# Optimization experiments

Hardware: AMD Instinct MI355X
Metric: run time of the kernel (lower is better)

Reference implementation:

```python
import jax, jax.numpy as jnp
import numpy as np

NUMBASIS = 10
OFFSET = jnp.linspace(-3.0, 3.0, NUMBASIS)
COEFF = -0.5 / (OFFSET[1] - OFFSET[0]) ** 2
CR_CR_MEAN, CR_CR_STD = 4.0, 0.16
CR_I_MEAN, CR_I_STD = 2.8, 0.035
ANGLE_MEAN, ANGLE_STD = -0.025, 0.06

E, N, G = 1_000_000, 250_000, 512

def _rbf(x):
    # x: [E, 1] -> [E, NUMBASIS]; PyG GaussianSmearing
    d = x - OFFSET
    return jnp.exp(COEFF * d * d)

def _layernorm(x, g, b, eps=1e-5):
    mu = jnp.mean(x, axis=-1, keepdims=True)
    xc = x - mu
    var = jnp.mean(xc * xc, axis=-1, keepdims=True)
    return xc * jax.lax.rsqrt(var + eps) * g + b

def setup_inputs() -> dict:
    key = jax.random.key(0)
    ks = jax.random.split(key, 16)
    def w(k, shape):
        return jax.random.normal(k, shape, jnp.float32) / np.sqrt(shape[0])
    return {
        "edge_src": jax.random.randint(ks[0], (E,), 0, N),
        "edge_dst": jax.random.randint(ks[1], (E,), 0, N),
        "batch_idx": jnp.sort(jax.random.randint(ks[2], (N,), 0, G)),
        "cell": jax.random.normal(ks[3], (G, 3, 3), jnp.float32),
        "edge_shift": jax.random.normal(ks[4], (E, 3), jnp.float32),
        "pos": jax.random.normal(ks[5], (N, 3), jnp.float32),
        "angles": jax.random.normal(ks[6], (E,), jnp.float32),
        "cr_i_bonds": jax.random.normal(ks[7], (E, 4), jnp.float32),
        "ln_g": jnp.ones((60,), jnp.float32),
        "ln_b": jnp.zeros((60,), jnp.float32),
        "wn1": w(ks[8], (60, 32)), "bn1": jnp.zeros((32,), jnp.float32),
        "wn2": w(ks[9], (32, 1)), "bn2": jnp.zeros((1,), jnp.float32),
        "we1": w(ks[10], (60, 64)), "be1": jnp.zeros((64,), jnp.float32),
        "we2": w(ks[11], (64, 1)), "be2": jnp.zeros((1,), jnp.float32),
        "wr1": w(ks[12], (60, 32)), "br1": jnp.zeros((32,), jnp.float32),
        "wr2": w(ks[13], (32, 2)), "br2": jnp.zeros((2,), jnp.float32),
    }

def reference(edge_src, edge_dst, batch_idx, cell, edge_shift, pos, angles,
              cr_i_bonds, ln_g, ln_b, wn1, bn1, wn2, bn2, we1, be1, we2, be2,
              wr1, br1, wr2, br2):
    gidx = batch_idx[edge_src]                      # [E]
    bcell = cell[gidx]                              # [E,3,3]
    tvec = jnp.einsum('ei,eij->ej', edge_shift, bcell)
    radvec = pos[edge_dst] - pos[edge_src] + tvec   # [E,3]
    dist = jnp.linalg.norm(radvec, axis=1, keepdims=True)  # [E,1]
    ang = angles.reshape(-1, 1)
    dist_z = (dist - CR_CR_MEAN) / CR_CR_STD
    ang_z = (ang - ANGLE_MEAN) / ANGLE_STD
    legs_z = (cr_i_bonds - CR_I_MEAN) / CR_I_STD    # [E,4]
    emb = jnp.concatenate([
        _rbf(dist_z), _rbf(ang_z),
        _rbf(legs_z[:, 0:1]), _rbf(legs_z[:, 1:2]),
        _rbf(legs_z[:, 2:3]), _rbf(legs_z[:, 3:4]),
    ], axis=-1)                                     # [E,60]
    h = _layernorm(emb, ln_g, ln_b)
    # dropout layers are identity in eval mode
    routing = jax.nn.softmax(jax.nn.silu(h @ wr1 + br1) @ wr2 + br2, axis=-1)
    pred_normal = jax.nn.silu(h @ wn1 + bn1) @ wn2 + bn2   # [E,1]
    pred_extreme = jax.nn.silu(h @ we1 + be1) @ we2 + be2  # [E,1]
    out = routing[:, 0:1] * pred_normal + routing[:, 1:2] * pred_extreme
    return out.reshape(-1)
```

## Files before the change

### kernel.cpp

```cpp
#include <hip/hip_runtime.h>
#include <math.h>

#define E_THREADS 256
#define EPB 256

typedef __attribute__((ext_vector_type(8))) short short8;
typedef __attribute__((ext_vector_type(4))) float floatx4;


__device__ __constant__ float c_B[10] = {
    -9.7397680f, -7.5753751f, -5.4109822f, -3.2465893f, -1.0821964f,
     1.0821964f,  3.2465893f,  5.4109822f,  7.5753751f,  9.7397680f
};
__device__ __constant__ float c_C[10] = {
    -14.609652f, -8.8378534f, -4.5091519f, -1.6232946f, -0.18036607f,
    -0.18036607f, -1.6232946f, -4.5091519f, -8.8378534f, -14.609652f
};

__device__ inline unsigned short f2bf(float f) {
    union { float f; unsigned u; } v; v.f = f;
    unsigned r = v.u + 0x7FFFu + ((v.u >> 16) & 1u);
    return (unsigned short)(r >> 16);
}

__device__ inline unsigned cvt_pk_bf16(float lo, float hi) {
    unsigned r;
    asm("v_cvt_pk_bf16_f32 %0, %1, %2" : "=v"(r) : "v"(lo), "v"(hi));
    return r;
}

__device__ inline float fexp2(float x) { return __builtin_amdgcn_exp2f(x); }
__device__ inline float frcp(float x)  { return __builtin_amdgcn_rcpf(x); }
#define LOG2E 1.44269504f

__global__ __launch_bounds__(256)
void prep_weights(
    const float* __restrict__ ln_g, const float* __restrict__ ln_b,
    const float* __restrict__ wn1, const float* __restrict__ bn1,
    const float* __restrict__ wn2, const float* __restrict__ bn2,
    const float* __restrict__ we1, const float* __restrict__ be1,
    const float* __restrict__ we2, const float* __restrict__ be2,
    const float* __restrict__ wr1, const float* __restrict__ br1,
    const float* __restrict__ wr2, const float* __restrict__ br2,
    char* __restrict__ ws)
{
    uint4* WF  = (uint4*)ws;
    float* W2A = (float*)(ws + 16384);
    float* W2B = (float*)(ws + 16896);
    float* SC  = (float*)(ws + 17024);
    const int tid = threadIdx.x;

    for (int idx = tid; idx < 1024; idx += 256) {
        int u = idx >> 7, s = (idx >> 6) & 1, lane = idx & 63;
        int lcol = lane & 15, khi = lane >> 4;
        int n = 16 * u + lcol;
        int kbase = s * 32 + khi * 8;
        float w8[8];
        for (int j = 0; j < 8; ++j) {
            int k = kbase + j;
            float w = 0.0f;
            if (k < 60) {
                float wv = (n < 32) ? wn1[k * 32 + n]
                         : (n < 96) ? we1[k * 64 + (n - 32)]
                                    : wr1[k * 32 + (n - 96)];
                w = ln_g[k] * wv;
            } else if (k == 60) {
                float b = (n < 32) ? bn1[n] : (n < 96) ? be1[n - 32] : br1[n - 96];
                for (int kk = 0; kk < 60; ++kk) {
                    float wv = (n < 32) ? wn1[kk * 32 + n]
                             : (n < 96) ? we1[kk * 64 + (n - 32)]
                                        : wr1[kk * 32 + (n - 96)];
                    b += ln_b[kk] * wv;
                }
                w = b;
            }
            w8[j] = w;
        }
        unsigned q0 = (unsigned)f2bf(w8[0]) | ((unsigned)f2bf(w8[1]) << 16);
        unsigned q1 = (unsigned)f2bf(w8[2]) | ((unsigned)f2bf(w8[3]) << 16);
        unsigned q2 = (unsigned)f2bf(w8[4]) | ((unsigned)f2bf(w8[5]) << 16);
        unsigned q3 = (unsigned)f2bf(w8[6]) | ((unsigned)f2bf(w8[7]) << 16);
        WF[idx] = make_uint4(q0, q1, q2, q3);
    }
    if (tid < 128) {
        int n = tid;
        W2A[n] = (n < 32) ? wn2[n] : (n < 96) ? we2[n - 32] : wr2[(n - 96) * 2];
    }
    if (tid >= 128 && tid < 160) W2B[tid - 128] = wr2[(tid - 128) * 2 + 1];
    if (tid == 0) { SC[0] = bn2[0]; SC[1] = be2[0]; SC[2] = br2[0]; SC[3] = br2[1]; }
}

__attribute__((amdgpu_waves_per_eu(4, 4)))
__global__ __launch_bounds__(E_THREADS, 4)
void exchange_block_kernel(
    const int*   __restrict__ edge_src,
    const int*   __restrict__ edge_dst,
    const int*   __restrict__ batch_idx,
    const float* __restrict__ cell,
    const float* __restrict__ edge_shift,
    const float* __restrict__ pos,
    const float* __restrict__ angles,
    const float* __restrict__ cr_bonds,
    const char*  __restrict__ ws,
    float* __restrict__ out, int E)
{
    __shared__ __align__(16) unsigned short HLDS[EPB * 64];
    __shared__ __align__(16) float LW2A[128];
    __shared__ __align__(16) float LW2B[32];

    const int tid = threadIdx.x;
    const int e = blockIdx.x * EPB + tid;

    if (tid < 128)                LW2A[tid] = ((const float*)(ws + 16384))[tid];
    else if (tid < 160)           LW2B[tid - 128] = ((const float*)(ws + 16896))[tid - 128];

    float h[64];
    if (e < E) {
        int s = edge_src[e];
        int d = edge_dst[e];
        int g = batch_idx[s];
        float sh0 = edge_shift[e * 3 + 0];
        float sh1 = edge_shift[e * 3 + 1];
        float sh2 = edge_shift[e * 3 + 2];
        const float* c = cell + g * 9;
        float t0 = sh0 * c[0] + sh1 * c[3] + sh2 * c[6];
        float t1 = sh0 * c[1] + sh1 * c[4] + sh2 * c[7];
        float t2 = sh0 * c[2] + sh1 * c[5] + sh2 * c[8];
        float r0 = pos[d * 3 + 0] - pos[s * 3 + 0] + t0;
        float r1 = pos[d * 3 + 1] - pos[s * 3 + 1] + t1;
        float r2 = pos[d * 3 + 2] - pos[s * 3 + 2] + t2;
        float dist = sqrtf(r0 * r0 + r1 * r1 + r2 * r2);

        float z[6];
        z[0] = (dist - 4.0f) * (1.0f / 0.16f);
        z[1] = (angles[e] + 0.025f) * (1.0f / 0.06f);
        z[2] = (cr_bonds[e * 4 + 0] - 2.8f) * (1.0f / 0.035f);
        z[3] = (cr_bonds[e * 4 + 1] - 2.8f) * (1.0f / 0.035f);
        z[4] = (cr_bonds[e * 4 + 2] - 2.8f) * (1.0f / 0.035f);
        z[5] = (cr_bonds[e * 4 + 3] - 2.8f) * (1.0f / 0.035f);

        #pragma unroll
        for (int gi = 0; gi < 6; ++gi) {
            float zv = z[gi];
            float az2 = -1.6232946f * zv * zv;
            #pragma unroll
            for (int k = 0; k < 10; ++k)
                h[gi * 10 + k] = fexp2(az2 + fmaf(zv, c_B[k], c_C[k]));
        }
        float mu = 0.0f;
        #pragma unroll
        for (int k = 0; k < 60; ++k) mu += h[k];
        mu *= (1.0f / 60.0f);
        float var = 0.0f;
        #pragma unroll
        for (int k = 0; k < 60; ++k) { float xc = h[k] - mu; var += xc * xc; }
        var *= (1.0f / 60.0f);
        float rs = rsqrtf(var + 1e-5f);
        float nmurs = -mu * rs;
        #pragma unroll
        for (int k = 0; k < 60; ++k) h[k] = fmaf(h[k], rs, nmurs);
    } else {
        #pragma unroll
        for (int k = 0; k < 60; ++k) h[k] = 0.0f;
    }
    h[60] = 1.0f;
    h[61] = 0.0f; h[62] = 0.0f; h[63] = 0.0f;

    {
        const int swz = (tid & 7) << 4;
        #pragma unroll
        for (int c = 0; c < 8; ++c) {
            unsigned q0 = cvt_pk_bf16(h[8 * c + 0], h[8 * c + 1]);
            unsigned q1 = cvt_pk_bf16(h[8 * c + 2], h[8 * c + 3]);
            unsigned q2 = cvt_pk_bf16(h[8 * c + 4], h[8 * c + 5]);
            unsigned q3 = cvt_pk_bf16(h[8 * c + 6], h[8 * c + 7]);
            *(uint4*)((char*)HLDS + tid * 128 + ((c * 16) ^ swz)) = make_uint4(q0, q1, q2, q3);
        }
    }
    __syncthreads();

    const uint4* WF = (const uint4*)ws;
    const float* SC = (const float*)(ws + 17024);

    const int lane = tid & 63;
    const int wv   = tid >> 6;
    const int lcol = lane & 15;
    const int khi  = lane >> 4;
    const int kof  = khi * 16;

    uint4 wf[16];
    #pragma unroll
    for (int i = 0; i < 16; ++i) wf[i] = WF[i * 64 + lane];

    const float bn2v = SC[0], be2v = SC[1], br2v0 = SC[2], br2v1 = SC[3];

    #pragma unroll
    for (int t = 0; t < 4; ++t) {
        const int hrow = wv * 64 + t * 16 + lcol;
        const char* hbase = (const char*)HLDS + hrow * 128;
        const int hswz = (hrow & 7) << 4;
        short8 b0 = *(const short8*)(hbase + ((0  + kof) ^ hswz));
        short8 b1 = *(const short8*)(hbase + ((64 + kof) ^ hswz));

        float sN = 0.0f, sE = 0.0f, sR0 = 0.0f, sR1 = 0.0f;
        #pragma unroll
        for (int u = 0; u < 8; ++u) {
            short8 a0 = *(const short8*)&wf[u * 2 + 0];
            short8 a1 = *(const short8*)&wf[u * 2 + 1];
            floatx4 acc = (floatx4){0.0f, 0.0f, 0.0f, 0.0f};
            acc = __builtin_amdgcn_mfma_f32_16x16x32_bf16(a0, b0, acc, 0, 0, 0);
            acc = __builtin_amdgcn_mfma_f32_16x16x32_bf16(a1, b1, acc, 0, 0, 0);

            float4 w2 = *(const float4*)&LW2A[16 * u + khi * 4];
            const float* w2p = (const float*)&w2;
            float4 wb4;
            const float* wbp = (const float*)&wb4;
            if (u >= 6) wb4 = *(const float4*)&LW2B[(u - 6) * 16 + khi * 4];
            #pragma unroll
            for (int j = 0; j < 4; ++j) {
                float a  = acc[j];
                float sl = a * frcp(1.0f + fexp2(a * -LOG2E));
                float w  = w2p[j];
                if (u < 2)      sN += sl * w;
                else if (u < 6) sE += sl * w;
                else {
                    sR0 += sl * w;
                    sR1 += sl * wbp[j];
                }
            }
        }
        sN  += __shfl_xor(sN,  16); sN  += __shfl_xor(sN,  32);
        sE  += __shfl_xor(sE,  16); sE  += __shfl_xor(sE,  32);
        sR0 += __shfl_xor(sR0, 16); sR0 += __shfl_xor(sR0, 32);
        sR1 += __shfl_xor(sR1, 16); sR1 += __shfl_xor(sR1, 32);

        sN += bn2v; sE += be2v; sR0 += br2v0; sR1 += br2v1;
        float rt = frcp(1.0f + fexp2((sR1 - sR0) * LOG2E));
        float val = sE + rt * (sN - sE);

        if (lane < 16) {
            int eb = blockIdx.x * EPB + wv * 64 + t * 16 + lcol;
            if (eb < E) out[eb] = val;
        }
    }
}

extern "C" void kernel_launch(void* const* d_in, const int* in_sizes, int n_in,
                              void* d_out, int out_size, void* d_ws, size_t ws_size,
                              hipStream_t stream)
{
    const int*   edge_src  = (const int*)  d_in[0];
    const int*   edge_dst  = (const int*)  d_in[1];
    const int*   batch_idx = (const int*)  d_in[2];
    const float* cell      = (const float*)d_in[3];
    const float* edge_shift= (const float*)d_in[4];
    const float* pos       = (const float*)d_in[5];
    const float* angles    = (const float*)d_in[6];
    const float* cr_bonds  = (const float*)d_in[7];
    const float* ln_g      = (const float*)d_in[8];
    const float* ln_b      = (const float*)d_in[9];
    const float* wn1 = (const float*)d_in[10]; const float* bn1 = (const float*)d_in[11];
    const float* wn2 = (const float*)d_in[12]; const float* bn2 = (const float*)d_in[13];
    const float* we1 = (const float*)d_in[14]; const float* be1 = (const float*)d_in[15];
    const float* we2 = (const float*)d_in[16]; const float* be2 = (const float*)d_in[17];
    const float* wr1 = (const float*)d_in[18]; const float* br1 = (const float*)d_in[19];
    const float* wr2 = (const float*)d_in[20]; const float* br2 = (const float*)d_in[21];

    int E = in_sizes[0];
    float* out = (float*)d_out;

    hipLaunchKernelGGL(prep_weights, dim3(1), dim3(256), 0, stream,
                       ln_g, ln_b, wn1, bn1, wn2, bn2, we1, be1, we2, be2,
                       wr1, br1, wr2, br2, (char*)d_ws);

    int grid = (E + EPB - 1) / EPB;
    hipLaunchKernelGGL(exchange_block_kernel, dim3(grid), dim3(E_THREADS), 0, stream,
                       edge_src, edge_dst, batch_idx, cell, edge_shift, pos,
                       angles, cr_bonds, (const char*)d_ws, out, E);
}
```

Before: 82.19 us.

## Compute Gaussian RBF via exp recurrence and halve block size

Replaces the ten exp2 evaluations per basis group with two exp2 calls plus a multiplicative recurrence (ratio between consecutive Gaussians is itself geometric), clamping z to keep the products finite. Block size drops from 256 to 128 edges with an adjusted waves-per-EU hint, and an empty asm barrier pins the preloaded weight fragments in registers. The recurrence cuts transcendental instruction count but can accumulate rounding error and changes underflow behaviour for extreme z.

```diff
diff --git a/kernel.cpp b/kernel.cpp
--- a/kernel.cpp
+++ b/kernel.cpp
@@ -1,21 +1,14 @@
 #include <hip/hip_runtime.h>
 #include <math.h>
 
-#define E_THREADS 256
-#define EPB 256
+#define E_THREADS 128
+#define EPB 128
 
 typedef __attribute__((ext_vector_type(8))) short short8;
 typedef __attribute__((ext_vector_type(4))) float floatx4;
 
 
-__device__ __constant__ float c_B[10] = {
-    -9.7397680f, -7.5753751f, -5.4109822f, -3.2465893f, -1.0821964f,
-     1.0821964f,  3.2465893f,  5.4109822f,  7.5753751f,  9.7397680f
-};
-__device__ __constant__ float c_C[10] = {
-    -14.609652f, -8.8378534f, -4.5091519f, -1.6232946f, -0.18036607f,
-    -0.18036607f, -1.6232946f, -4.5091519f, -8.8378534f, -14.609652f
-};
+#define A_L2E 1.6230319f
 
 __device__ inline unsigned short f2bf(float f) {
     union { float f; unsigned u; } v; v.f = f;
@@ -90,7 +83,7 @@
     if (tid == 0) { SC[0] = bn2[0]; SC[1] = be2[0]; SC[2] = br2[0]; SC[3] = br2[1]; }
 }
 
-__attribute__((amdgpu_waves_per_eu(4, 4)))
+__attribute__((amdgpu_waves_per_eu(4, 5)))
 __global__ __launch_bounds__(E_THREADS, 4)
 void exchange_block_kernel(
     const int*   __restrict__ edge_src,
@@ -111,8 +104,8 @@
     const int tid = threadIdx.x;
     const int e = blockIdx.x * EPB + tid;
 
-    if (tid < 128)                LW2A[tid] = ((const float*)(ws + 16384))[tid];
-    else if (tid < 160)           LW2B[tid - 128] = ((const float*)(ws + 16896))[tid - 128];
+    LW2A[tid] = ((const float*)(ws + 16384))[tid];
+    if (tid < 32) LW2B[tid] = ((const float*)(ws + 16896))[tid];
 
     float h[64];
     if (e < E) {
@@ -141,11 +134,17 @@
 
         #pragma unroll
         for (int gi = 0; gi < 6; ++gi) {
-            float zv = z[gi];
-            float az2 = -1.6232946f * zv * zv;
+            float zv = fminf(13.0f, fmaxf(-13.0f, z[gi]));
+            float tt = zv + 3.0f;
+            float hv = fexp2(-A_L2E * tt * tt);
+            float rv = fexp2(fmaf(zv, 2.1640426f, 5.7707802f));
+            h[gi * 10] = hv;
             #pragma unroll
-            for (int k = 0; k < 10; ++k)
-                h[gi * 10 + k] = fexp2(az2 + fmaf(zv, c_B[k], c_C[k]));
+            for (int k = 1; k < 10; ++k) {
+                hv *= rv;
+                rv *= 0.36787944f;
+                h[gi * 10 + k] = hv;
+            }
         }
         float mu = 0.0f;
         #pragma unroll
@@ -191,6 +190,9 @@
     uint4 wf[16];
     #pragma unroll
     for (int i = 0; i < 16; ++i) wf[i] = WF[i * 64 + lane];
+    #pragma unroll
+    for (int i = 0; i < 16; ++i)
+        asm volatile("" : "+v"(wf[i].x), "+v"(wf[i].y), "+v"(wf[i].z), "+v"(wf[i].w));
 
     const float bn2v = SC[0], be2v = SC[1], br2v0 = SC[2], br2v1 = SC[3];
 
```

After: 83.70 us. Within noise of the previous version (+1.8%).
